# Performance work log

Hardware: AMD Instinct MI355X
Metric: run time of the kernel (lower is better)

## Reference

```python
import jax, jax.numpy as jnp
import numpy as np

N_SAMPLES = 32768
N_EVENTS = 16
WINDOW = 512
STEP = 256
N_FRAMES = 128          # n_samples // step_size
TOTAL_COEFFS = 16385    # n_samples // 2 + 1
N_COEFFS = 257          # window_size // 2 + 1
MIN_RES = 0.01


def max_norm(x):
    return x / (jnp.max(jnp.abs(x), axis=-1, keepdims=True) + 1e-8)


def linear_interp_last(x, out_size):
    """torch F.interpolate(mode='linear', align_corners=False) along last dim."""
    L = x.shape[-1]
    scale = L / out_size
    pos = (jnp.arange(out_size, dtype=jnp.float32) + 0.5) * scale - 0.5
    pos = jnp.clip(pos, 0.0, L - 1.0)
    i0 = jnp.floor(pos).astype(jnp.int32)
    i1 = jnp.minimum(i0 + 1, L - 1)
    w = pos - i0.astype(jnp.float32)
    return x[..., i0] * (1.0 - w) + x[..., i1] * w


def setup_inputs() -> dict:
    key = jax.random.key(0)
    k1, k2 = jax.random.split(key)
    x = jax.random.uniform(k1, (32, N_EVENTS, 533), dtype=jnp.float32)
    noise = jax.random.uniform(k2, (32, N_EVENTS, N_SAMPLES), dtype=jnp.float32)
    return {"x": x, "noise": noise}


def _forward(x, noise):
    x = jnp.clip(x, 0.0, 1.0)  # unit_activation

    # unpack
    means = x[..., 0:1] * 2.0 - 1.0                       # [B,E,1]
    stds = x[..., 1:2] * 0.1                              # [B,E,1]
    amps = x[..., 2:3]                                    # [B,E,1]
    res_mag = MIN_RES + (1.0 - MIN_RES) * x[..., 3:260]   # [B,E,257]
    freqs = (jnp.fft.rfftfreq(WINDOW) * np.pi).astype(jnp.float32)
    res_phase = x[..., 260:517] * (2.0 * np.pi) - np.pi + freqs  # [B,E,257]
    noise_coeff = x[..., 517:533]                         # [B,E,16]

    # ---- localized_noise ----
    rng = jnp.arange(N_SAMPLES, dtype=jnp.float32)
    mu = jnp.clip(means * N_SAMPLES, -(N_SAMPLES // 2), N_SAMPLES * 1.5)
    sigma = jnp.clip((1e-8 + stds) * N_SAMPLES, 0.0, N_SAMPLES - 1.0)
    logp = -0.5 * ((rng - mu) / sigma) ** 2 - jnp.log(sigma) - 0.5 * np.log(2.0 * np.pi)
    probs = max_norm(jnp.exp(logp))                       # [B,E,N]

    u = noise * 2.0 - 1.0                                 # uniform(-1,1)
    spec_shape = linear_interp_last(noise_coeff, TOTAL_COEFFS)  # [B,E,16385]
    nspec = jnp.fft.rfft(u, norm='ortho') * spec_shape
    nband = jnp.fft.irfft(nspec, n=N_SAMPLES, norm='ortho')
    atoms = probs * nband * amps                          # [B,E,N]

    # ---- resonance ----
    padded = jnp.pad(atoms, ((0, 0), (0, 0), (0, STEP)))
    idx = jnp.arange(N_FRAMES)[:, None] * STEP + jnp.arange(WINDOW)[None, :]
    frames = padded[..., idx]                             # [B,E,F,W]
    n = jnp.arange(WINDOW, dtype=jnp.float32)
    hamming = 0.54 - 0.46 * jnp.cos(2.0 * np.pi * n / WINDOW)  # periodic
    spec = jnp.fft.rfft(frames * hamming, norm='ortho')   # [B,E,F,257]

    # to_mag_and_phase
    re, im = spec.real, spec.imag
    mag = jnp.sqrt(re * re + im * im) + 1e-8              # [B,E,F,257]
    phase = (im / mag) * np.pi

    # mag recurrence m_t = mag_t + r * m_{t-1} (m_0 = mag_0) via scan over frames
    mag_t = jnp.moveaxis(mag, 2, 0)                       # [F,B,E,C]
    def step(carry, a):
        m = a + res_mag * carry
        return m, m
    _, ms = jax.lax.scan(step, jnp.zeros_like(mag_t[0]), mag_t)
    mags = jnp.moveaxis(ms, 0, 2)                         # [B,E,F,C]

    # phase: frame 0 unchanged, frames>=1 get + res_phase offset
    fmask = (jnp.arange(N_FRAMES) > 0).astype(phase.dtype)[None, None, :, None]
    phases = phase + fmask * res_phase[:, :, None, :]

    final = jax.lax.complex(mags * jnp.cos(phases), mags * jnp.sin(phases))
    res = jnp.fft.irfft(final, n=WINDOW, norm='ortho')    # [B,E,F,W]

    # overlap-add (hop = W/2), no window
    firsts, seconds = res[..., :STEP], res[..., STEP:]
    out = jnp.zeros(res.shape[:2] + (N_FRAMES + 1, STEP), res.dtype)
    out = out.at[:, :, :N_FRAMES].add(firsts).at[:, :, 1:].add(seconds)
    sig = out.reshape(out.shape[0], out.shape[1], -1)[..., :N_SAMPLES]  # [B,E,N]

    summed = jnp.sum(sig, axis=1, keepdims=True)          # [B,1,N]
    return max_norm(summed)


def reference(x, noise):
    return _forward(x, noise)
```

## Files before the change

kernel.cpp:

```cpp
#include <hip/hip_runtime.h>
#include <math.h>

#define PI_F 3.14159265358979323846f

__device__ __forceinline__ float2 cadd(float2 a, float2 b){ return make_float2(a.x+b.x, a.y+b.y); }
__device__ __forceinline__ float2 csub(float2 a, float2 b){ return make_float2(a.x-b.x, a.y-b.y); }
__device__ __forceinline__ float2 cmul(float2 a, float2 b){ return make_float2(a.x*b.x - a.y*b.y, a.x*b.y + a.y*b.x); }
__device__ __forceinline__ float2 cscale(float2 a, float s){ return make_float2(a.x*s, a.y*s); }
__device__ __forceinline__ float clip01(float v){ return fminf(fmaxf(v, 0.0f), 1.0f); }

__device__ __forceinline__ float uniformf(float v){
  return __int_as_float(__builtin_amdgcn_readfirstlane(__float_as_int(v)));
}

__device__ __forceinline__ int swz14(int p){ return p ^ (15 & ((p>>4) ^ (p>>8) ^ (p>>12))); }
__device__ __forceinline__ int swz8 (int p){ return p ^ ((p>>4) & 15); }

__device__ __forceinline__ int dr14(int k){
  unsigned x = __brev((unsigned)k) >> 18;
  return (int)(((x & 0x1555u) << 1) | ((x >> 1) & 0x1555u));
}
__device__ __forceinline__ int dr8(int k){
  unsigned x = __brev((unsigned)k) >> 24;
  return (int)(((x & 0x55u) << 1) | ((x >> 1) & 0x55u));
}

__device__ __forceinline__ void unpack_pair(float2 Zk, float2 Zm, float sn, float cs,
                                            float2& Uk, float2& Um) {
  float2 A  = make_float2(0.5f*(Zk.x+Zm.x), 0.5f*(Zk.y-Zm.y));
  float2 B  = make_float2(Zk.x-Zm.x, Zk.y+Zm.y);
  Uk = cadd(A, cmul(B, make_float2(-0.5f*sn, -0.5f*cs)));
  float2 Bm = make_float2(-B.x, B.y);
  Um = cadd(make_float2(A.x, -A.y), cmul(Bm, make_float2(-0.5f*sn, 0.5f*cs)));
}
__device__ __forceinline__ void repack_pair(float2 Vk, float2 Vm, float sn, float cs,
                                            float2& Wk, float2& Wm) {
  float2 P = make_float2(Vk.x+Vm.x, Vk.y-Vm.y);
  float2 Q = make_float2(Vk.x-Vm.x, Vk.y+Vm.y);
  Wk = cscale(cadd(P, cmul(Q, make_float2(-sn, cs))), 0.5f);
  float2 Qm = make_float2(-Q.x, Q.y);
  Wm = cscale(cadd(make_float2(P.x, -P.y), cmul(Qm, make_float2(-sn, -cs))), 0.5f);
}

__device__ __forceinline__ float sshape(int k, const float* ncs) {
  float pos = ((float)k + 0.5f) * (16.0f/16385.0f) - 0.5f;
  pos = fminf(fmaxf(pos, 0.0f), 15.0f);
  float fi = floorf(pos);
  int i0 = (int)fi;
  int i1 = min(i0 + 1, 15);
  float w = pos - fi;
  return ncs[i0]*(1.0f-w) + ncs[i1]*w;
}

#define LGKM() asm volatile("s_waitcnt lgkmcnt(0)" ::: "memory")

__device__ __forceinline__ void big_stage_fwd(float2* Cb, int u, int J, int lj) {
  int j = u & (J-1);
  int base = ((u >> lj) << (lj+2)) | j;
  float2 a0 = Cb[swz14(base)];
  float2 a1 = Cb[swz14(base+J)];
  float2 a2 = Cb[swz14(base+2*J)];
  float2 a3 = Cb[swz14(base+3*J)];
  float sn, cs; __sincosf((float)j * (-PI_F/(2.0f*(float)J)), &sn, &cs);
  float2 w1 = make_float2(cs, sn), w2 = cmul(w1,w1), w3 = cmul(w2,w1);
  float2 t0 = cadd(a0,a2), t1 = cadd(a1,a3), t2 = csub(a0,a2), t3 = csub(a1,a3);
  float2 mi = make_float2(t3.y, -t3.x);
  Cb[swz14(base)]     = cadd(t0,t1);
  Cb[swz14(base+J)]   = cmul(cadd(t2,mi), w1);
  Cb[swz14(base+2*J)] = cmul(csub(t0,t1), w2);
  Cb[swz14(base+3*J)] = cmul(csub(t2,mi), w3);
}
__device__ __forceinline__ void big_stage_inv(float2* Cb, int u, int J, int lj) {
  int j = u & (J-1);
  int base = ((u >> lj) << (lj+2)) | j;
  float sn, cs; __sincosf((float)j * (PI_F/(2.0f*(float)J)), &sn, &cs);
  float2 v1 = make_float2(cs, sn), v2 = cmul(v1,v1), v3 = cmul(v2,v1);
  float2 b0 = Cb[swz14(base)];
  float2 b1 = cmul(Cb[swz14(base+J)],   v1);
  float2 b2 = cmul(Cb[swz14(base+2*J)], v2);
  float2 b3 = cmul(Cb[swz14(base+3*J)], v3);
  float2 s02 = cadd(b0,b2), d02 = csub(b0,b2), s13 = cadd(b1,b3), d13 = csub(b1,b3);
  float2 id13 = make_float2(-d13.y, d13.x);
  Cb[swz14(base)]     = cadd(s02, s13);
  Cb[swz14(base+J)]   = cadd(d02, id13);
  Cb[swz14(base+2*J)] = csub(s02, s13);
  Cb[swz14(base+3*J)] = csub(d02, id13);
}
__device__ __forceinline__ void fr_stage_fwd(float2* row, int u, int J, int lj) {
  int j = u & (J-1);
  int base = ((u >> lj) << (lj+2)) | j;
  float2 a0 = row[swz8(base)];
  float2 a1 = row[swz8(base+J)];
  float2 a2 = row[swz8(base+2*J)];
  float2 a3 = row[swz8(base+3*J)];
  float sn, cs; __sincosf((float)j * (-PI_F/(2.0f*(float)J)), &sn, &cs);
  float2 w1 = make_float2(cs, sn), w2 = cmul(w1,w1), w3 = cmul(w2,w1);
  float2 t0 = cadd(a0,a2), t1 = cadd(a1,a3), t2 = csub(a0,a2), t3 = csub(a1,a3);
  float2 mi = make_float2(t3.y, -t3.x);
  row[swz8(base)]     = cadd(t0,t1);
  row[swz8(base+J)]   = cmul(cadd(t2,mi), w1);
  row[swz8(base+2*J)] = cmul(csub(t0,t1), w2);
  row[swz8(base+3*J)] = cmul(csub(t2,mi), w3);
}
__device__ __forceinline__ void fr_stage_inv(float2* row, int u, int J, int lj) {
  int j = u & (J-1);
  int base = ((u >> lj) << (lj+2)) | j;
  float sn, cs; __sincosf((float)j * (PI_F/(2.0f*(float)J)), &sn, &cs);
  float2 v1 = make_float2(cs, sn), v2 = cmul(v1,v1), v3 = cmul(v2,v1);
  float2 b0 = row[swz8(base)];
  float2 b1 = cmul(row[swz8(base+J)],   v1);
  float2 b2 = cmul(row[swz8(base+2*J)], v2);
  float2 b3 = cmul(row[swz8(base+3*J)], v3);
  float2 s02 = cadd(b0,b2), d02 = csub(b0,b2), s13 = cadd(b1,b3), d13 = csub(b1,b3);
  float2 id13 = make_float2(-d13.y, d13.x);
  row[swz8(base)]     = cadd(s02, s13);
  row[swz8(base+J)]   = cadd(d02, id13);
  row[swz8(base+2*J)] = csub(s02, s13);
  row[swz8(base+3*J)] = csub(d02, id13);
}

__global__ void __launch_bounds__(1024, 1)
atoms_zero(float* __restrict__ out) { out[blockIdx.x * 1024 + threadIdx.x] = 0.0f; }

__global__ void __launch_bounds__(1024, 4)
atoms_noise(const float* __restrict__ x, const float* __restrict__ noise,
            float2* __restrict__ nbout) {
  const int blk = blockIdx.x;
  const int t   = threadIdx.x;

  const float* xr = x + (size_t)blk * 533;
  const float* nr = noise + (size_t)blk * 32768;

  __shared__ float2 Cs[16384];
  __shared__ float  ncs[16];

  if (t < 16) ncs[t] = clip01(xr[517 + t]);

  {
    const float4* nr4 = (const float4*)nr;
    #pragma unroll
    for (int i2 = 0; i2 < 8; ++i2) {
      int m = t + (i2 << 10);
      float4 v4 = nr4[m];
      Cs[swz14(2*m)]   = make_float2(v4.x*2.0f-1.0f, v4.y*2.0f-1.0f);
      Cs[swz14(2*m+1)] = make_float2(v4.z*2.0f-1.0f, v4.w*2.0f-1.0f);
    }
  }
  __syncthreads();

  const int ub = ((t >> 6) << 8) + (t & 63);

  #pragma unroll
  for (int r = 0; r < 4; ++r) big_stage_fwd(Cs, ub + (r<<6), 4096, 12);
  __syncthreads();
  #pragma unroll
  for (int r = 0; r < 4; ++r) big_stage_fwd(Cs, ub + (r<<6), 1024, 10);
  __syncthreads();
  #pragma unroll
  for (int r = 0; r < 4; ++r) big_stage_fwd(Cs, ub + (r<<6), 256, 8);
  LGKM();
  #pragma unroll
  for (int r = 0; r < 4; ++r) big_stage_fwd(Cs, ub + (r<<6), 64, 6);
  LGKM();
  #pragma unroll
  for (int r = 0; r < 4; ++r) big_stage_fwd(Cs, ub + (r<<6), 16, 4);
  LGKM();
  #pragma unroll
  for (int r = 0; r < 4; ++r) big_stage_fwd(Cs, ub + (r<<6), 4, 2);
  LGKM();
  #pragma unroll
  for (int r = 0; r < 4; ++r) big_stage_fwd(Cs, ub + (r<<6), 1, 0);
  __syncthreads();

  {
    const float invM = 1.0f / 16384.0f;
    for (int k = t; k < 8192; k += 1024) {
      if (k == 0) {
        float2 Z0 = Cs[0];
        float U0 = Z0.x + Z0.y;
        float UM = Z0.x - Z0.y;
        float V0 = U0 * sshape(0, ncs) * invM;
        float VM = UM * sshape(16384, ncs) * invM;
        Cs[0] = make_float2(0.5f*(V0+VM), 0.5f*(V0-VM));
      } else {
        int pk = swz14(dr14(k));
        int pm = swz14(dr14(16384 - k));
        float2 Zk = Cs[pk], Zm = Cs[pm];
        float sn, cs; __sincosf((float)k * (PI_F / 16384.0f), &sn, &cs);
        float2 Uk, Um; unpack_pair(Zk, Zm, sn, cs, Uk, Um);
        float2 Vk = cscale(Uk, sshape(k, ncs) * invM);
        float2 Vm = cscale(Um, sshape(16384 - k, ncs) * invM);
        float2 Wk, Wm; repack_pair(Vk, Vm, sn, cs, Wk, Wm);
        Cs[pk] = Wk; Cs[pm] = Wm;
      }
    }
    if (t == 0) {
      int p = swz14(2);
      float2 Z = Cs[p];
      float2 U = make_float2(Z.x, -Z.y);
      float2 V = cscale(U, sshape(8192, ncs) * invM);
      Cs[p] = make_float2(V.x, -V.y);
    }
  }
  __syncthreads();

  #pragma unroll
  for (int r = 0; r < 4; ++r) big_stage_inv(Cs, ub + (r<<6), 1, 0);
  LGKM();
  #pragma unroll
  for (int r = 0; r < 4; ++r) big_stage_inv(Cs, ub + (r<<6), 4, 2);
  LGKM();
  #pragma unroll
  for (int r = 0; r < 4; ++r) big_stage_inv(Cs, ub + (r<<6), 16, 4);
  LGKM();
  #pragma unroll
  for (int r = 0; r < 4; ++r) big_stage_inv(Cs, ub + (r<<6), 64, 6);
  LGKM();
  #pragma unroll
  for (int r = 0; r < 4; ++r) big_stage_inv(Cs, ub + (r<<6), 256, 8);
  __syncthreads();
  #pragma unroll
  for (int r = 0; r < 4; ++r) big_stage_inv(Cs, ub + (r<<6), 1024, 10);
  __syncthreads();
  #pragma unroll
  for (int r = 0; r < 4; ++r) big_stage_inv(Cs, ub + (r<<6), 4096, 12);
  __syncthreads();

  float2* dst = nbout + ((size_t)blk << 14);
  #pragma unroll
  for (int ii = 0; ii < 16; ++ii) {
    int j = t + (ii << 10);
    dst[j] = Cs[swz14(j)];
  }
}

__global__ void __launch_bounds__(512, 2)
atoms_frames(const float* __restrict__ x, const float2* __restrict__ nband,
             float2* __restrict__ wsrows) {
  const int blk = blockIdx.x;
  const int t   = threadIdx.x;
  const int w   = t >> 6;
  const int l   = t & 63;

  const float* xr = x + (size_t)blk * 533;
  const float2* nbd = nband + ((size_t)blk << 14);
  float2* wsrow = wsrows + ((size_t)blk << 14);

  __shared__ float2 FR[8][256];
  __shared__ float  magb[8*257];
  __shared__ float  resmag[257], resphase[257], msarr[257];
  __shared__ float2 carrybuf[2][128];
  __shared__ float2 hamtab[256];

  const float xc0 = clip01(xr[0]);
  const float xc1 = clip01(xr[1]);
  const float amp = clip01(xr[2]);
  const float mean = xc0 * 2.0f - 1.0f;
  const float stdv = xc1 * 0.1f;
  float mu_v = fminf(fmaxf(mean * 32768.0f, -16384.0f), 49152.0f);
  float sigma = fminf(fmaxf((1e-8f + stdv) * 32768.0f, 0.0f), 32767.0f);
  float K_v = -logf(sigma) - 0.91893853320467274f;
  float invsig_v = 1.0f / sigma;
  float istar = fminf(fmaxf(roundf(mu_v), 0.0f), 32767.0f);
  float ds0 = (istar - mu_v) * invsig_v;
  float emax = __expf(-0.5f * ds0 * ds0 + K_v);
  const float mu     = uniformf(mu_v);
  const float invsig = uniformf(invsig_v);
  const float K      = uniformf(K_v);
  const float gscale = uniformf(amp / (emax + 1e-8f));

  if (t < 257) {
    resmag[t]   = 0.01f + 0.99f * clip01(xr[3 + t]);
    resphase[t] = clip01(xr[260 + t]) * (2.0f*PI_F) - PI_F + (float)t * (PI_F / 512.0f);
    msarr[t]    = 0.0f;
  }
  if (t < 128) carrybuf[0][t] = make_float2(0.0f, 0.0f);
  if (t < 256) {
    const float W512 = 2.0f * PI_F / 512.0f;
    float n0 = (float)(2*t);
    hamtab[t] = make_float2(0.54f - 0.46f*__cosf(n0*W512),
                            0.54f - 0.46f*__cosf((n0+1.0f)*W512));
  }
  __syncthreads();

  const float C2 = 0.044194173824159216f;
  const float F2 = 0.08838834764831845f;
  float2* row = FR[w];

  for (int g = 0; g < 16; ++g) {
    #pragma unroll
    for (int rep = 0; rep < 4; ++rep) {
      int slot = t + (rep << 9);
      int i = slot >> 8, j = slot & 255;
      int fg = (g << 3) + i;
      int cidx = (fg << 7) + j;
      float2 v = make_float2(0.0f, 0.0f);
      if (cidx < 16384) {
        float2 nb = nbd[cidx];
        float s0 = (float)(2*cidx);
        float d0 = (s0 - mu) * invsig;
        float d1 = (s0 + 1.0f - mu) * invsig;
        float2 h = hamtab[j];
        v = make_float2(__expf(-0.5f*d0*d0 + K) * gscale * nb.x * h.x,
                        __expf(-0.5f*d1*d1 + K) * gscale * nb.y * h.y);
      }
      FR[i][swz8(j)] = v;
    }
    __syncthreads();

    {
      fr_stage_fwd(row, l, 64, 6); LGKM();
      fr_stage_fwd(row, l, 16, 4); LGKM();
      fr_stage_fwd(row, l, 4, 2);  LGKM();
      fr_stage_fwd(row, l, 1, 0);  LGKM();

      if (l == 0) {
        float2 Z0 = row[0];
        float U0 = Z0.x + Z0.y, UM = Z0.x - Z0.y;
        magb[w*257 + 0]   = fabsf(U0)*C2 + 1e-8f;
        magb[w*257 + 256] = fabsf(UM)*C2 + 1e-8f;
        float2 Z = row[swz8(2)];
        magb[w*257 + 128] = sqrtf(Z.x*Z.x + Z.y*Z.y)*C2 + 1e-8f;
      } else {
        int pk = swz8(dr8(l)), pm = swz8(dr8(256 - l));
        float sn, cs; __sincosf((float)l * (PI_F/256.0f), &sn, &cs);
        float2 Uk, Um; unpack_pair(row[pk], row[pm], sn, cs, Uk, Um);
        magb[w*257 + l]     = sqrtf(Uk.x*Uk.x + Uk.y*Uk.y)*C2 + 1e-8f;
        magb[w*257 + 256-l] = sqrtf(Um.x*Um.x + Um.y*Um.y)*C2 + 1e-8f;
      }
      {
        const int kB = l + 64;
        int pk = swz8(dr8(kB)), pm = swz8(dr8(256 - kB));
        float sn, cs; __sincosf((float)kB * (PI_F/256.0f), &sn, &cs);
        float2 Uk, Um; unpack_pair(row[pk], row[pm], sn, cs, Uk, Um);
        magb[w*257 + kB]     = sqrtf(Uk.x*Uk.x + Uk.y*Uk.y)*C2 + 1e-8f;
        magb[w*257 + 256-kB] = sqrtf(Um.x*Um.x + Um.y*Um.y)*C2 + 1e-8f;
      }
    }
    __syncthreads();

    if (t < 257) {
      float rm = resmag[t], r = msarr[t];
      #pragma unroll
      for (int i = 0; i < 8; ++i) {
        float mg = magb[i*257 + t];
        r = fmaf(rm, r, mg);
        magb[i*257 + t] = r;
      }
      msarr[t] = r;
    }
    __syncthreads();

    {
      float fm = ((g << 3) + w > 0) ? 1.0f : 0.0f;
      if (l == 0) {
        float ms0 = magb[w*257 + 0]   * F2;
        float msM = magb[w*257 + 256] * F2;
        float V0 = ms0 * __cosf(fm*resphase[0]);
        float VM = msM * __cosf(fm*resphase[256]);
        row[0] = make_float2(0.5f*(V0+VM), 0.5f*(V0-VM));
        float2 Z = row[swz8(2)];
        float2 U = make_float2(Z.x, -Z.y);
        float mC = sqrtf(U.x*U.x + U.y*U.y)*C2 + 1e-8f;
        float pC = (U.y*C2/mC)*PI_F + fm*resphase[128];
        float msC = magb[w*257 + 128] * F2;
        float sC, cC; __sincosf(pC, &sC, &cC);
        row[swz8(2)] = make_float2(msC*cC, -(msC*sC));
      } else {
        int pk = swz8(dr8(l)), pm = swz8(dr8(256 - l));
        float sn, cs; __sincosf((float)l * (PI_F/256.0f), &sn, &cs);
        float2 Uk, Um; unpack_pair(row[pk], row[pm], sn, cs, Uk, Um);
        float mk = sqrtf(Uk.x*Uk.x + Uk.y*Uk.y)*C2 + 1e-8f;
        float mm = sqrtf(Um.x*Um.x + Um.y*Um.y)*C2 + 1e-8f;
        float p1 = (Uk.y*C2/mk)*PI_F + fm*resphase[l];
        float p2 = (Um.y*C2/mm)*PI_F + fm*resphase[256-l];
        float msk = magb[w*257 + l]     * F2;
        float msm = magb[w*257 + 256-l] * F2;
        float s1,c1,s2,c2; __sincosf(p1,&s1,&c1); __sincosf(p2,&s2,&c2);
        float2 Vk = make_float2(msk*c1, msk*s1);
        float2 Vm = make_float2(msm*c2, msm*s2);
        float2 Wk, Wm; repack_pair(Vk, Vm, sn, cs, Wk, Wm);
        row[pk] = Wk; row[pm] = Wm;
      }
      {
        const int kB = l + 64;
        int pk = swz8(dr8(kB)), pm = swz8(dr8(256 - kB));
        float sn, cs; __sincosf((float)kB * (PI_F/256.0f), &sn, &cs);
        float2 Uk, Um; unpack_pair(row[pk], row[pm], sn, cs, Uk, Um);
        float mk = sqrtf(Uk.x*Uk.x + Uk.y*Uk.y)*C2 + 1e-8f;
        float mm = sqrtf(Um.x*Um.x + Um.y*Um.y)*C2 + 1e-8f;
        float p1 = (Uk.y*C2/mk)*PI_F + fm*resphase[kB];
        float p2 = (Um.y*C2/mm)*PI_F + fm*resphase[256-kB];
        float msk = magb[w*257 + kB]     * F2;
        float msm = magb[w*257 + 256-kB] * F2;
        float s1,c1,s2,c2; __sincosf(p1,&s1,&c1); __sincosf(p2,&s2,&c2);
        float2 Vk = make_float2(msk*c1, msk*s1);
        float2 Vm = make_float2(msm*c2, msm*s2);
        float2 Wk, Wm; repack_pair(Vk, Vm, sn, cs, Wk, Wm);
        row[pk] = Wk; row[pm] = Wm;
      }
      LGKM();
      fr_stage_inv(row, l, 1, 0);  LGKM();
      fr_stage_inv(row, l, 4, 2);  LGKM();
      fr_stage_inv(row, l, 16, 4); LGKM();
      fr_stage_inv(row, l, 64, 6);
    }
    __syncthreads();

    #pragma unroll
    for (int rep = 0; rep < 2; ++rep) {
      int slot = t + (rep << 9);
      int i = slot >> 7, j = slot & 127;
      int fg = (g << 3) + i;
      float2 first  = FR[i][swz8(j)];
      float2 second = (i > 0) ? FR[i-1][swz8(128 + j)] : carrybuf[g & 1][j];
      wsrow[(fg << 7) + j] = cadd(first, second);
      if (i == 7) {
        carrybuf[(g & 1) ^ 1][j] = FR[7][swz8(128 + j)];
      }
    }
    __syncthreads();
  }
}

__global__ void __launch_bounds__(1024, 4)
atoms_main(const float* __restrict__ x, const float* __restrict__ noise,
           float* __restrict__ outacc, float2* __restrict__ wsbuf, int use_ws) {
  const int blk = blockIdx.x;
  const int b   = blk >> 4;
  const int t   = threadIdx.x;
  const int w   = t >> 6;
  const int l   = t & 63;

  const float* xr = x + (size_t)blk * 533;
  const float* nr = noise + (size_t)blk * 32768;

  __shared__ float2 Cs[16384];
  __shared__ float2 FR[8][256];
  __shared__ float  magb[8*257];
  __shared__ float  resmag[257], resphase[257], msarr[257];
  __shared__ float2 carrybuf[2][128];
  __shared__ float2 hamtab[256];
  __shared__ float  ncs[16];

  const float xc0 = clip01(xr[0]);
  const float xc1 = clip01(xr[1]);
  const float amp = clip01(xr[2]);
  const float mean = xc0 * 2.0f - 1.0f;
  const float stdv = xc1 * 0.1f;
  float mu_v = fminf(fmaxf(mean * 32768.0f, -16384.0f), 49152.0f);
  float sigma = fminf(fmaxf((1e-8f + stdv) * 32768.0f, 0.0f), 32767.0f);
  float K_v = -logf(sigma) - 0.91893853320467274f;
  float invsig_v = 1.0f / sigma;
  float istar = fminf(fmaxf(roundf(mu_v), 0.0f), 32767.0f);
  float ds0 = (istar - mu_v) * invsig_v;
  float emax = __expf(-0.5f * ds0 * ds0 + K_v);
  const float mu     = uniformf(mu_v);
  const float invsig = uniformf(invsig_v);
  const float K      = uniformf(K_v);
  const float gscale = uniformf(amp / (emax + 1e-8f));

  if (t < 257) {
    resmag[t]   = 0.01f + 0.99f * clip01(xr[3 + t]);
    resphase[t] = clip01(xr[260 + t]) * (2.0f*PI_F) - PI_F + (float)t * (PI_F / 512.0f);
    msarr[t]    = 0.0f;
  }
  if (t < 16)  ncs[t] = clip01(xr[517 + t]);
  if (t < 128) carrybuf[0][t] = make_float2(0.0f, 0.0f);
  if (t < 256) {
    const float W512 = 2.0f * PI_F / 512.0f;
    float n0 = (float)(2*t);
    hamtab[t] = make_float2(0.54f - 0.46f*__cosf(n0*W512),
                            0.54f - 0.46f*__cosf((n0+1.0f)*W512));
  }

  {
    const float4* nr4 = (const float4*)nr;
    #pragma unroll
    for (int i2 = 0; i2 < 8; ++i2) {
      int m = t + (i2 << 10);
      float4 v4 = nr4[m];
      Cs[swz14(2*m)]   = make_float2(v4.x*2.0f-1.0f, v4.y*2.0f-1.0f);
      Cs[swz14(2*m+1)] = make_float2(v4.z*2.0f-1.0f, v4.w*2.0f-1.0f);
    }
  }
  __syncthreads();

  const int ub = ((t >> 6) << 8) + (t & 63);

  #pragma unroll
  for (int r = 0; r < 4; ++r) big_stage_fwd(Cs, ub + (r<<6), 4096, 12);
  __syncthreads();
  #pragma unroll
  for (int r = 0; r < 4; ++r) big_stage_fwd(Cs, ub + (r<<6), 1024, 10);
  __syncthreads();
  #pragma unroll
  for (int r = 0; r < 4; ++r) big_stage_fwd(Cs, ub + (r<<6), 256, 8);
  LGKM();
  #pragma unroll
  for (int r = 0; r < 4; ++r) big_stage_fwd(Cs, ub + (r<<6), 64, 6);
  LGKM();
  #pragma unroll
  for (int r = 0; r < 4; ++r) big_stage_fwd(Cs, ub + (r<<6), 16, 4);
  LGKM();
  #pragma unroll
  for (int r = 0; r < 4; ++r) big_stage_fwd(Cs, ub + (r<<6), 4, 2);
  LGKM();
  #pragma unroll
  for (int r = 0; r < 4; ++r) big_stage_fwd(Cs, ub + (r<<6), 1, 0);
  __syncthreads();

  {
    const float invM = 1.0f / 16384.0f;
    for (int k = t; k < 8192; k += 1024) {
      if (k == 0) {
        float2 Z0 = Cs[0];
        float U0 = Z0.x + Z0.y;
        float UM = Z0.x - Z0.y;
        float V0 = U0 * sshape(0, ncs) * invM;
        float VM = UM * sshape(16384, ncs) * invM;
        Cs[0] = make_float2(0.5f*(V0+VM), 0.5f*(V0-VM));
      } else {
        int pk = swz14(dr14(k));
        int pm = swz14(dr14(16384 - k));
        float2 Zk = Cs[pk], Zm = Cs[pm];
        float sn, cs; __sincosf((float)k * (PI_F / 16384.0f), &sn, &cs);
        float2 Uk, Um; unpack_pair(Zk, Zm, sn, cs, Uk, Um);
        float2 Vk = cscale(Uk, sshape(k, ncs) * invM);
        float2 Vm = cscale(Um, sshape(16384 - k, ncs) * invM);
        float2 Wk, Wm; repack_pair(Vk, Vm, sn, cs, Wk, Wm);
        Cs[pk] = Wk; Cs[pm] = Wm;
      }
    }
    if (t == 0) {
      int p = swz14(2);
      float2 Z = Cs[p];
      float2 U = make_float2(Z.x, -Z.y);
      float2 V = cscale(U, sshape(8192, ncs) * (1.0f/16384.0f));
      Cs[p] = make_float2(V.x, -V.y);
    }
  }
  __syncthreads();

  #pragma unroll
  for (int r = 0; r < 4; ++r) big_stage_inv(Cs, ub + (r<<6), 1, 0);
  LGKM();
  #pragma unroll
  for (int r = 0; r < 4; ++r) big_stage_inv(Cs, ub + (r<<6), 4, 2);
  LGKM();
  #pragma unroll
  for (int r = 0; r < 4; ++r) big_stage_inv(Cs, ub + (r<<6), 16, 4);
  LGKM();
  #pragma unroll
  for (int r = 0; r < 4; ++r) big_stage_inv(Cs, ub + (r<<6), 64, 6);
  LGKM();
  #pragma unroll
  for (int r = 0; r < 4; ++r) big_stage_inv(Cs, ub + (r<<6), 256, 8);
  __syncthreads();
  #pragma unroll
  for (int r = 0; r < 4; ++r) big_stage_inv(Cs, ub + (r<<6), 1024, 10);
  __syncthreads();
  #pragma unroll
  for (int r = 0; r < 4; ++r) big_stage_inv(Cs, ub + (r<<6), 4096, 12);
  __syncthreads();

  const float C2 = 0.044194173824159216f;
  const float F2 = 0.08838834764831845f;
  float2* row = (w < 8) ? FR[w] : FR[0];
  float2* wsrow = use_ws ? (wsbuf + ((size_t)blk << 14)) : (float2*)0;

  for (int g = 0; g < 16; ++g) {
    #pragma unroll
    for (int rep = 0; rep < 2; ++rep) {
      int slot = t + (rep << 10);
      int i = slot >> 8, j = slot & 255;
      int fg = (g << 3) + i;
      int cidx = (fg << 7) + j;
      float2 v = make_float2(0.0f, 0.0f);
      if (cidx < 16384) {
        float2 nb = Cs[swz14(cidx)];
        float s0 = (float)(2*cidx);
        float d0 = (s0 - mu) * invsig;
        float d1 = (s0 + 1.0f - mu) * invsig;
        float2 h = hamtab[j];
        v = make_float2(__expf(-0.5f*d0*d0 + K) * gscale * nb.x * h.x,
                        __expf(-0.5f*d1*d1 + K) * gscale * nb.y * h.y);
      }
      FR[i][swz8(j)] = v;
    }
    __syncthreads();

    if (w < 8) {
      fr_stage_fwd(row, l, 64, 6); LGKM();
      fr_stage_fwd(row, l, 16, 4); LGKM();
      fr_stage_fwd(row, l, 4, 2);  LGKM();
      fr_stage_fwd(row, l, 1, 0);  LGKM();

      if (l == 0) {
        float2 Z0 = row[0];
        float U0 = Z0.x + Z0.y, UM = Z0.x - Z0.y;
        magb[w*257 + 0]   = fabsf(U0)*C2 + 1e-8f;
        magb[w*257 + 256] = fabsf(UM)*C2 + 1e-8f;
        float2 Z = row[swz8(2)];
        magb[w*257 + 128] = sqrtf(Z.x*Z.x + Z.y*Z.y)*C2 + 1e-8f;
      } else {
        int pk = swz8(dr8(l)), pm = swz8(dr8(256 - l));
        float sn, cs; __sincosf((float)l * (PI_F/256.0f), &sn, &cs);
        float2 Uk, Um; unpack_pair(row[pk], row[pm], sn, cs, Uk, Um);
        magb[w*257 + l]     = sqrtf(Uk.x*Uk.x + Uk.y*Uk.y)*C2 + 1e-8f;
        magb[w*257 + 256-l] = sqrtf(Um.x*Um.x + Um.y*Um.y)*C2 + 1e-8f;
      }
      {
        const int kB = l + 64;
        int pk = swz8(dr8(kB)), pm = swz8(dr8(256 - kB));
        float sn, cs; __sincosf((float)kB * (PI_F/256.0f), &sn, &cs);
        float2 Uk, Um; unpack_pair(row[pk], row[pm], sn, cs, Uk, Um);
        magb[w*257 + kB]     = sqrtf(Uk.x*Uk.x + Uk.y*Uk.y)*C2 + 1e-8f;
        magb[w*257 + 256-kB] = sqrtf(Um.x*Um.x + Um.y*Um.y)*C2 + 1e-8f;
      }
    }
    __syncthreads();

    if (t < 257) {
      float rm = resmag[t], r = msarr[t];
      #pragma unroll
      for (int i = 0; i < 8; ++i) {
        float mg = magb[i*257 + t];
        r = fmaf(rm, r, mg);
        magb[i*257 + t] = r;
      }
      msarr[t] = r;
    }
    __syncthreads();

    if (w < 8) {
      float fm = ((g << 3) + w > 0) ? 1.0f : 0.0f;
      if (l == 0) {
        float ms0 = magb[w*257 + 0]   * F2;
        float msM = magb[w*257 + 256] * F2;
        float V0 = ms0 * __cosf(fm*resphase[0]);
        float VM = msM * __cosf(fm*resphase[256]);
        row[0] = make_float2(0.5f*(V0+VM), 0.5f*(V0-VM));
        float2 Z = row[swz8(2)];
        float2 U = make_float2(Z.x, -Z.y);
        float mC = sqrtf(U.x*U.x + U.y*U.y)*C2 + 1e-8f;
        float pC = (U.y*C2/mC)*PI_F + fm*resphase[128];
        float msC = magb[w*257 + 128] * F2;
        float sC, cC; __sincosf(pC, &sC, &cC);
        row[swz8(2)] = make_float2(msC*cC, -(msC*sC));
      } else {
        int pk = swz8(dr8(l)), pm = swz8(dr8(256 - l));
        float sn, cs; __sincosf((float)l * (PI_F/256.0f), &sn, &cs);
        float2 Uk, Um; unpack_pair(row[pk], row[pm], sn, cs, Uk, Um);
        float mk = sqrtf(Uk.x*Uk.x + Uk.y*Uk.y)*C2 + 1e-8f;
        float mm = sqrtf(Um.x*Um.x + Um.y*Um.y)*C2 + 1e-8f;
        float p1 = (Uk.y*C2/mk)*PI_F + fm*resphase[l];
        float p2 = (Um.y*C2/mm)*PI_F + fm*resphase[256-l];
        float msk = magb[w*257 + l]     * F2;
        float msm = magb[w*257 + 256-l] * F2;
        float s1,c1,s2,c2; __sincosf(p1,&s1,&c1); __sincosf(p2,&s2,&c2);
        float2 Vk = make_float2(msk*c1, msk*s1);
        float2 Vm = make_float2(msm*c2, msm*s2);
        float2 Wk, Wm; repack_pair(Vk, Vm, sn, cs, Wk, Wm);
        row[pk] = Wk; row[pm] = Wm;
      }
      {
        const int kB = l + 64;
        int pk = swz8(dr8(kB)), pm = swz8(dr8(256 - kB));
        float sn, cs; __sincosf((float)kB * (PI_F/256.0f), &sn, &cs);
        float2 Uk, Um; unpack_pair(row[pk], row[pm], sn, cs, Uk, Um);
        float mk = sqrtf(Uk.x*Uk.x + Uk.y*Uk.y)*C2 + 1e-8f;
        float mm = sqrtf(Um.x*Um.x + Um.y*Um.y)*C2 + 1e-8f;
        float p1 = (Uk.y*C2/mk)*PI_F + fm*resphase[kB];
        float p2 = (Um.y*C2/mm)*PI_F + fm*resphase[256-kB];
        float msk = magb[w*257 + kB]     * F2;
        float msm = magb[w*257 + 256-kB] * F2;
        float s1,c1,s2,c2; __sincosf(p1,&s1,&c1); __sincosf(p2,&s2,&c2);
        float2 Vk = make_float2(msk*c1, msk*s1);
        float2 Vm = make_float2(msm*c2, msm*s2);
        float2 Wk, Wm; repack_pair(Vk, Vm, sn, cs, Wk, Wm);
        row[pk] = Wk; row[pm] = Wm;
      }
      LGKM();
      fr_stage_inv(row, l, 1, 0);  LGKM();
      fr_stage_inv(row, l, 4, 2);  LGKM();
      fr_stage_inv(row, l, 16, 4); LGKM();
      fr_stage_inv(row, l, 64, 6);
    }
    __syncthreads();

    {
      int i = t >> 7, j = t & 127;
      int fg = (g << 3) + i;
      float2 first  = FR[i][swz8(j)];
      float2 second = (i > 0) ? FR[i-1][swz8(128 + j)] : carrybuf[g & 1][j];
      float2 v = cadd(first, second);
      if (use_ws) {
        wsrow[(fg << 7) + j] = v;
      } else {
        float* dst = outacc + (size_t)b*32768 + (fg << 8) + 2*j;
        atomicAdd(dst,     v.x);
        atomicAdd(dst + 1, v.y);
      }
      if (i == 7) {
        carrybuf[(g & 1) ^ 1][j] = FR[7][swz8(128 + j)];
      }
    }
    __syncthreads();
  }
}

__global__ void __launch_bounds__(1024, 1)
atoms_sum_max(const float* __restrict__ ws, float* __restrict__ out, float* __restrict__ wmax) {
  int blk = blockIdx.x;
  int b = blk >> 3, seg = blk & 7, tid = threadIdx.x;
  const float* base = ws + (size_t)b*16*32768 + (size_t)seg*4096;
  float v[4]; float m = 0.0f;
  #pragma unroll
  for (int i = 0; i < 4; ++i) {
    int idx = (i << 10) + tid;
    float s = 0.0f;
    #pragma unroll
    for (int e = 0; e < 16; ++e) s += base[(size_t)e*32768 + idx];
    v[i] = s; m = fmaxf(m, fabsf(s));
  }
  float* op = out + (size_t)b*32768 + (seg << 12);
  #pragma unroll
  for (int i = 0; i < 4; ++i) op[(i<<10) + tid] = v[i];
  __shared__ float red[1024];
  red[tid] = m; __syncthreads();
  for (int s2 = 512; s2 > 0; s2 >>= 1) {
    if (tid < s2) red[tid] = fmaxf(red[tid], red[tid + s2]);
    __syncthreads();
  }
  if (tid == 0) wmax[blk] = red[0];
}

__global__ void __launch_bounds__(1024, 1)
atoms_scale(float* __restrict__ out, const float* __restrict__ wmax) {
  int blk = blockIdx.x;
  int b = blk >> 3, seg = blk & 7, tid = threadIdx.x;
  const float* wm = wmax + b*8;
  float m = fmaxf(fmaxf(fmaxf(wm[0],wm[1]), fmaxf(wm[2],wm[3])),
                  fmaxf(fmaxf(wm[4],wm[5]), fmaxf(wm[6],wm[7])));
  float inv = 1.0f / (m + 1e-8f);
  float* op = out + (size_t)b*32768 + (seg << 12);
  #pragma unroll
  for (int i = 0; i < 4; ++i) op[(i<<10) + tid] *= inv;
}

__global__ void __launch_bounds__(1024, 1)
atoms_norm(float* __restrict__ out) {
  const int b = blockIdx.x;
  const int tid = threadIdx.x;
  float* p = out + (size_t)b * 32768;
  __shared__ float red[1024];
  float m = 0.0f;
  for (int i = tid; i < 32768; i += 1024) m = fmaxf(m, fabsf(p[i]));
  red[tid] = m;
  __syncthreads();
  for (int s = 512; s > 0; s >>= 1) {
    if (tid < s) red[tid] = fmaxf(red[tid], red[tid + s]);
    __syncthreads();
  }
  const float inv = 1.0f / (red[0] + 1e-8f);
  for (int i = tid; i < 32768; i += 1024) p[i] = p[i] * inv;
}

extern "C" void kernel_launch(void* const* d_in, const int* in_sizes, int n_in,
                              void* d_out, int out_size, void* d_ws, size_t ws_size,
                              hipStream_t stream) {
  (void)in_sizes; (void)n_in; (void)out_size;
  const float* x     = (const float*)d_in[0];
  const float* noise = (const float*)d_in[1];
  float* out = (float*)d_out;

  const size_t rows_f    = 512ull * 32768ull;
  const size_t need_ws    = rows_f*4 + 4096;
  const size_t need_split = rows_f*4 + 4096 + rows_f*4;

  if (d_ws != nullptr && ws_size >= need_split) {
    float* ws    = (float*)d_ws;
    float* wmax  = ws + rows_f;
    float2* nbd  = (float2*)(ws + rows_f + 1024);
    atoms_noise <<<512, 1024, 0, stream>>>(x, noise, nbd);
    atoms_frames<<<512,  512, 0, stream>>>(x, nbd, (float2*)ws);
    atoms_sum_max<<<256, 1024, 0, stream>>>(ws, out, wmax);
    atoms_scale<<<256, 1024, 0, stream>>>(out, wmax);
  } else if (d_ws != nullptr && ws_size >= need_ws) {
    float* ws = (float*)d_ws;
    float* wmax = ws + rows_f;
    atoms_main<<<512, 1024, 0, stream>>>(x, noise, nullptr, (float2*)ws, 1);
    atoms_sum_max<<<256, 1024, 0, stream>>>(ws, out, wmax);
    atoms_scale<<<256, 1024, 0, stream>>>(out, wmax);
  } else {
    atoms_zero<<<1024, 1024, 0, stream>>>(out);
    atoms_main<<<512, 1024, 0, stream>>>(x, noise, out, nullptr, 0);
    atoms_norm<<<32, 1024, 0, stream>>>(out);
  }
}
```

Before: 274.2 us.

## Process two frames per wave in atoms_frames, halving group iterations and barriers

```diff
diff --git a/kernel.cpp b/kernel.cpp
--- a/kernel.cpp
+++ b/kernel.cpp
@@ -86,6 +86,52 @@
   Cb[swz14(base+2*J)] = csub(s02, s13);
   Cb[swz14(base+3*J)] = csub(d02, id13);
 }
+
+__device__ __forceinline__ void fr2_fwd(float2* rowA, float2* rowB, int l, int J, int lj) {
+  int j = l & (J-1);
+  int base = ((l >> lj) << (lj+2)) | j;
+  int i0 = swz8(base), i1 = swz8(base+J), i2 = swz8(base+2*J), i3 = swz8(base+3*J);
+  float2 a0=rowA[i0], a1=rowA[i1], a2=rowA[i2], a3=rowA[i3];
+  float2 b0=rowB[i0], b1=rowB[i1], b2=rowB[i2], b3=rowB[i3];
+  float sn, cs; __sincosf((float)j * (-PI_F/(2.0f*(float)J)), &sn, &cs);
+  float2 w1 = make_float2(cs, sn), w2 = cmul(w1,w1), w3 = cmul(w2,w1);
+  {
+    float2 t0=cadd(a0,a2), t1=cadd(a1,a3), t2=csub(a0,a2), t3=csub(a1,a3);
+    float2 mi=make_float2(t3.y,-t3.x);
+    rowA[i0]=cadd(t0,t1);          rowA[i1]=cmul(cadd(t2,mi),w1);
+    rowA[i2]=cmul(csub(t0,t1),w2); rowA[i3]=cmul(csub(t2,mi),w3);
+  }
+  {
+    float2 t0=cadd(b0,b2), t1=cadd(b1,b3), t2=csub(b0,b2), t3=csub(b1,b3);
+    float2 mi=make_float2(t3.y,-t3.x);
+    rowB[i0]=cadd(t0,t1);          rowB[i1]=cmul(cadd(t2,mi),w1);
+    rowB[i2]=cmul(csub(t0,t1),w2); rowB[i3]=cmul(csub(t2,mi),w3);
+  }
+}
+__device__ __forceinline__ void fr2_inv(float2* rowA, float2* rowB, int l, int J, int lj) {
+  int j = l & (J-1);
+  int base = ((l >> lj) << (lj+2)) | j;
+  int i0 = swz8(base), i1 = swz8(base+J), i2 = swz8(base+2*J), i3 = swz8(base+3*J);
+  float2 a0=rowA[i0], a1=rowA[i1], a2=rowA[i2], a3=rowA[i3];
+  float2 b0=rowB[i0], b1=rowB[i1], b2=rowB[i2], b3=rowB[i3];
+  float sn, cs; __sincosf((float)j * (PI_F/(2.0f*(float)J)), &sn, &cs);
+  float2 v1 = make_float2(cs, sn), v2 = cmul(v1,v1), v3 = cmul(v2,v1);
+  {
+    float2 c1=cmul(a1,v1), c2=cmul(a2,v2), c3=cmul(a3,v3);
+    float2 s02=cadd(a0,c2), d02=csub(a0,c2), s13=cadd(c1,c3), d13=csub(c1,c3);
+    float2 id13=make_float2(-d13.y,d13.x);
+    rowA[i0]=cadd(s02,s13); rowA[i1]=cadd(d02,id13);
+    rowA[i2]=csub(s02,s13); rowA[i3]=csub(d02,id13);
+  }
+  {
+    float2 c1=cmul(b1,v1), c2=cmul(b2,v2), c3=cmul(b3,v3);
+    float2 s02=cadd(b0,c2), d02=csub(b0,c2), s13=cadd(c1,c3), d13=csub(c1,c3);
+    float2 id13=make_float2(-d13.y,d13.x);
+    rowB[i0]=cadd(s02,s13); rowB[i1]=cadd(d02,id13);
+    rowB[i2]=csub(s02,s13); rowB[i3]=csub(d02,id13);
+  }
+}
+
 __device__ __forceinline__ void fr_stage_fwd(float2* row, int u, int J, int lj) {
   int j = u & (J-1);
   int base = ((u >> lj) << (lj+2)) | j;
@@ -234,7 +280,7 @@
   }
 }
 
-__global__ void __launch_bounds__(512, 2)
+__global__ void __launch_bounds__(512, 4)
 atoms_frames(const float* __restrict__ x, const float2* __restrict__ nband,
              float2* __restrict__ wsrows) {
   const int blk = blockIdx.x;
@@ -246,8 +292,9 @@
   const float2* nbd = nband + ((size_t)blk << 14);
   float2* wsrow = wsrows + ((size_t)blk << 14);
 
-  __shared__ float2 FR[8][256];
-  __shared__ float  magb[8*257];
+  __shared__ float2 FR[16][256];
+  __shared__ float  magb[16*257];
+  __shared__ float  phb[16*257];
   __shared__ float  resmag[257], resphase[257], msarr[257];
   __shared__ float2 carrybuf[2][128];
   __shared__ float2 hamtab[256];
@@ -285,138 +332,193 @@
 
   const float C2 = 0.044194173824159216f;
   const float F2 = 0.08838834764831845f;
-  float2* row = FR[w];
-
-  for (int g = 0; g < 16; ++g) {
+  const int iA = 2*w, iB = 2*w + 1;
+  float2* rowA = FR[iA];
+  float2* rowB = FR[iB];
+
+  for (int g = 0; g < 8; ++g) {
+    const int fgA = (g << 4) + iA;
+    const int fgB = fgA + 1;
+
     #pragma unroll
-    for (int rep = 0; rep < 4; ++rep) {
-      int slot = t + (rep << 9);
-      int i = slot >> 8, j = slot & 255;
-      int fg = (g << 3) + i;
-      int cidx = (fg << 7) + j;
-      float2 v = make_float2(0.0f, 0.0f);
-      if (cidx < 16384) {
-        float2 nb = nbd[cidx];
-        float s0 = (float)(2*cidx);
-        float d0 = (s0 - mu) * invsig;
-        float d1 = (s0 + 1.0f - mu) * invsig;
-        float2 h = hamtab[j];
-        v = make_float2(__expf(-0.5f*d0*d0 + K) * gscale * nb.x * h.x,
-                        __expf(-0.5f*d1*d1 + K) * gscale * nb.y * h.y);
-      }
-      FR[i][swz8(j)] = v;
-    }
-    __syncthreads();
-
-    {
-      fr_stage_fwd(row, l, 64, 6); LGKM();
-      fr_stage_fwd(row, l, 16, 4); LGKM();
-      fr_stage_fwd(row, l, 4, 2);  LGKM();
-      fr_stage_fwd(row, l, 1, 0);  LGKM();
-
-      if (l == 0) {
+    for (int r = 0; r < 4; ++r) {
+      int j = l + (r << 6);
+      float2 h = hamtab[j];
+      {
+        int cidx = (fgA << 7) + j;
+        float2 v = make_float2(0.0f, 0.0f);
+        if (cidx < 16384) {
+          float2 nb = nbd[cidx];
+          float s0 = (float)(2*cidx);
+          float d0 = (s0 - mu) * invsig;
+          float d1 = (s0 + 1.0f - mu) * invsig;
+          v = make_float2(__expf(-0.5f*d0*d0 + K) * gscale * nb.x * h.x,
+                          __expf(-0.5f*d1*d1 + K) * gscale * nb.y * h.y);
+        }
+        rowA[swz8(j)] = v;
+      }
+      {
+        int cidx = (fgB << 7) + j;
+        float2 v = make_float2(0.0f, 0.0f);
+        if (cidx < 16384) {
+          float2 nb = nbd[cidx];
+          float s0 = (float)(2*cidx);
+          float d0 = (s0 - mu) * invsig;
+          float d1 = (s0 + 1.0f - mu) * invsig;
+          v = make_float2(__expf(-0.5f*d0*d0 + K) * gscale * nb.x * h.x,
+                          __expf(-0.5f*d1*d1 + K) * gscale * nb.y * h.y);
+        }
+        rowB[swz8(j)] = v;
+      }
+    }
+    LGKM();
+
+    fr2_fwd(rowA, rowB, l, 64, 6); LGKM();
+    fr2_fwd(rowA, rowB, l, 16, 4); LGKM();
+    fr2_fwd(rowA, rowB, l, 4, 2);  LGKM();
+    fr2_fwd(rowA, rowB, l, 1, 0);  LGKM();
+
+    if (l == 0) {
+      #pragma unroll
+      for (int s = 0; s < 2; ++s) {
+        float2* row = s ? rowB : rowA;
+        int ii = s ? iB : iA;
         float2 Z0 = row[0];
         float U0 = Z0.x + Z0.y, UM = Z0.x - Z0.y;
-        magb[w*257 + 0]   = fabsf(U0)*C2 + 1e-8f;
-        magb[w*257 + 256] = fabsf(UM)*C2 + 1e-8f;
+        magb[ii*257 + 0]   = fabsf(U0)*C2 + 1e-8f;
+        magb[ii*257 + 256] = fabsf(UM)*C2 + 1e-8f;
         float2 Z = row[swz8(2)];
-        magb[w*257 + 128] = sqrtf(Z.x*Z.x + Z.y*Z.y)*C2 + 1e-8f;
+        float2 U = make_float2(Z.x, -Z.y);
+        float mC = sqrtf(U.x*U.x + U.y*U.y)*C2 + 1e-8f;
+        magb[ii*257 + 128] = mC;
+        phb[ii*257 + 128]  = (U.y*C2/mC)*PI_F;
+      }
+    } else {
+      int pk = swz8(dr8(l)), pm = swz8(dr8(256 - l));
+      float sn, cs; __sincosf((float)l * (PI_F/256.0f), &sn, &cs);
+      #pragma unroll
+      for (int s = 0; s < 2; ++s) {
+        float2* row = s ? rowB : rowA;
+        int ii = s ? iB : iA;
+        float2 Uk, Um; unpack_pair(row[pk], row[pm], sn, cs, Uk, Um);
+        float mk = sqrtf(Uk.x*Uk.x + Uk.y*Uk.y)*C2 + 1e-8f;
+        float mm = sqrtf(Um.x*Um.x + Um.y*Um.y)*C2 + 1e-8f;
+        magb[ii*257 + l]     = mk;
+        magb[ii*257 + 256-l] = mm;
+        phb[ii*257 + l]      = (Uk.y*C2/mk)*PI_F;
+        phb[ii*257 + 256-l]  = (Um.y*C2/mm)*PI_F;
+      }
+    }
+    {
+      const int kB = l + 64;
+      int pk = swz8(dr8(kB)), pm = swz8(dr8(256 - kB));
+      float sn, cs; __sincosf((float)kB * (PI_F/256.0f), &sn, &cs);
+      #pragma unroll
+      for (int s = 0; s < 2; ++s) {
+        float2* row = s ? rowB : rowA;
+        int ii = s ? iB : iA;
+        float2 Uk, Um; unpack_pair(row[pk], row[pm], sn, cs, Uk, Um);
+        float mk = sqrtf(Uk.x*Uk.x + Uk.y*Uk.y)*C2 + 1e-8f;
+        float mm = sqrtf(Um.x*Um.x + Um.y*Um.y)*C2 + 1e-8f;
+        magb[ii*257 + kB]     = mk;
+        magb[ii*257 + 256-kB] = mm;
+        phb[ii*257 + kB]      = (Uk.y*C2/mk)*PI_F;
+        phb[ii*257 + 256-kB]  = (Um.y*C2/mm)*PI_F;
+      }
+    }
+    __syncthreads();
+
+    if (t < 257) {
+      float rm = resmag[t], r = msarr[t];
+      float mg[16];
+      #pragma unroll
+      for (int i = 0; i < 16; ++i) mg[i] = magb[i*257 + t];
+      #pragma unroll
+      for (int i = 0; i < 16; ++i) {
+        r = fmaf(rm, r, mg[i]);
+        magb[i*257 + t] = r;
+      }
+      msarr[t] = r;
+    }
+    __syncthreads();
+
+    {
+      const float fmA = (fgA > 0) ? 1.0f : 0.0f;
+      if (l == 0) {
+        #pragma unroll
+        for (int s = 0; s < 2; ++s) {
+          float2* row = s ? rowB : rowA;
+          int ii = s ? iB : iA;
+          float fm = s ? 1.0f : fmA;
+          float ms0 = magb[ii*257 + 0]   * F2;
+          float msM = magb[ii*257 + 256] * F2;
+          float V0 = ms0 * __cosf(fm*resphase[0]);
+          float VM = msM * __cosf(fm*resphase[256]);
+          row[0] = make_float2(0.5f*(V0+VM), 0.5f*(V0-VM));
+          float msC = magb[ii*257 + 128] * F2;
+          float pC  = phb[ii*257 + 128] + fm*resphase[128];
+          float sC, cC; __sincosf(pC, &sC, &cC);
+          row[swz8(2)] = make_float2(msC*cC, -(msC*sC));
+        }
       } else {
         int pk = swz8(dr8(l)), pm = swz8(dr8(256 - l));
         float sn, cs; __sincosf((float)l * (PI_F/256.0f), &sn, &cs);
-        float2 Uk, Um; unpack_pair(row[pk], row[pm], sn, cs, Uk, Um);
-        magb[w*257 + l]     = sqrtf(Uk.x*Uk.x + Uk.y*Uk.y)*C2 + 1e-8f;
-        magb[w*257 + 256-l] = sqrtf(Um.x*Um.x + Um.y*Um.y)*C2 + 1e-8f;
+        float rp1 = resphase[l], rp2 = resphase[256-l];
+        #pragma unroll
+        for (int s = 0; s < 2; ++s) {
+          float2* row = s ? rowB : rowA;
+          int ii = s ? iB : iA;
+          float fm = s ? 1.0f : fmA;
+          float msk = magb[ii*257 + l]     * F2;
+          float msm = magb[ii*257 + 256-l] * F2;
+          float p1 = phb[ii*257 + l]     + fm*rp1;
+          float p2 = phb[ii*257 + 256-l] + fm*rp2;
+          float s1,c1,s2,c2; __sincosf(p1,&s1,&c1); __sincosf(p2,&s2,&c2);
+          float2 Vk = make_float2(msk*c1, msk*s1);
+          float2 Vm = make_float2(msm*c2, msm*s2);
+          float2 Wk, Wm; repack_pair(Vk, Vm, sn, cs, Wk, Wm);
+          row[pk] = Wk; row[pm] = Wm;
+        }
       }
       {
         const int kB = l + 64;
         int pk = swz8(dr8(kB)), pm = swz8(dr8(256 - kB));
         float sn, cs; __sincosf((float)kB * (PI_F/256.0f), &sn, &cs);
-        float2 Uk, Um; unpack_pair(row[pk], row[pm], sn, cs, Uk, Um);
-        magb[w*257 + kB]     = sqrtf(Uk.x*Uk.x + Uk.y*Uk.y)*C2 + 1e-8f;
-        magb[w*257 + 256-kB] = sqrtf(Um.x*Um.x + Um.y*Um.y)*C2 + 1e-8f;
-      }
-    }
-    __syncthreads();
-
-    if (t < 257) {
-      float rm = resmag[t], r = msarr[t];
-      #pragma unroll
-      for (int i = 0; i < 8; ++i) {
-        float mg = magb[i*257 + t];
-        r = fmaf(rm, r, mg);
-        magb[i*257 + t] = r;
-      }
-      msarr[t] = r;
-    }
-    __syncthreads();
-
-    {
-      float fm = ((g << 3) + w > 0) ? 1.0f : 0.0f;
-      if (l == 0) {
-        float ms0 = magb[w*257 + 0]   * F2;
-        float msM = magb[w*257 + 256] * F2;
-        float V0 = ms0 * __cosf(fm*resphase[0]);
-        float VM = msM * __cosf(fm*resphase[256]);
-        row[0] = make_float2(0.5f*(V0+VM), 0.5f*(V0-VM));
-        float2 Z = row[swz8(2)];
-        float2 U = make_float2(Z.x, -Z.y);
-        float mC = sqrtf(U.x*U.x + U.y*U.y)*C2 + 1e-8f;
-        float pC = (U.y*C2/mC)*PI_F + fm*resphase[128];
-        float msC = magb[w*257 + 128] * F2;
-        float sC, cC; __sincosf(pC, &sC, &cC);
-        row[swz8(2)] = make_float2(msC*cC, -(msC*sC));
-      } else {
-        int pk = swz8(dr8(l)), pm = swz8(dr8(256 - l));
-        float sn, cs; __sincosf((float)l * (PI_F/256.0f), &sn, &cs);
-        float2 Uk, Um; unpack_pair(row[pk], row[pm], sn, cs, Uk, Um);
-        float mk = sqrtf(Uk.x*Uk.x + Uk.y*Uk.y)*C2 + 1e-8f;
-        float mm = sqrtf(Um.x*Um.x + Um.y*Um.y)*C2 + 1e-8f;
-        float p1 = (Uk.y*C2/mk)*PI_F + fm*resphase[l];
-        float p2 = (Um.y*C2/mm)*PI_F + fm*resphase[256-l];
-        float msk = magb[w*257 + l]     * F2;
-        float msm = magb[w*257 + 256-l] * F2;
-        float s1,c1,s2,c2; __sincosf(p1,&s1,&c1); __sincosf(p2,&s2,&c2);
-        float2 Vk = make_float2(msk*c1, msk*s1);
-        float2 Vm = make_float2(msm*c2, msm*s2);
-        float2 Wk, Wm; repack_pair(Vk, Vm, sn, cs, Wk, Wm);
-        row[pk] = Wk; row[pm] = Wm;
-      }
-      {
-        const int kB = l + 64;
-        int pk = swz8(dr8(kB)), pm = swz8(dr8(256 - kB));
-        float sn, cs; __sincosf((float)kB * (PI_F/256.0f), &sn, &cs);
-        float2 Uk, Um; unpack_pair(row[pk], row[pm], sn, cs, Uk, Um);
-        float mk = sqrtf(Uk.x*Uk.x + Uk.y*Uk.y)*C2 + 1e-8f;
-        float mm = sqrtf(Um.x*Um.x + Um.y*Um.y)*C2 + 1e-8f;
-        float p1 = (Uk.y*C2/mk)*PI_F + fm*resphase[kB];
-        float p2 = (Um.y*C2/mm)*PI_F + fm*resphase[256-kB];
-        float msk = magb[w*257 + kB]     * F2;
-        float msm = magb[w*257 + 256-kB] * F2;
-        float s1,c1,s2,c2; __sincosf(p1,&s1,&c1); __sincosf(p2,&s2,&c2);
-        float2 Vk = make_float2(msk*c1, msk*s1);
-        float2 Vm = make_float2(msm*c2, msm*s2);
-        float2 Wk, Wm; repack_pair(Vk, Vm, sn, cs, Wk, Wm);
-        row[pk] = Wk; row[pm] = Wm;
+        float rp1 = resphase[kB], rp2 = resphase[256-kB];
+        #pragma unroll
+        for (int s = 0; s < 2; ++s) {
+          float2* row = s ? rowB : rowA;
+          int ii = s ? iB : iA;
+          float fm = s ? 1.0f : fmA;
+          float msk = magb[ii*257 + kB]     * F2;
+          float msm = magb[ii*257 + 256-kB] * F2;
+          float p1 = phb[ii*257 + kB]     + fm*rp1;
+          float p2 = phb[ii*257 + 256-kB] + fm*rp2;
+          float s1,c1,s2,c2; __sincosf(p1,&s1,&c1); __sincosf(p2,&s2,&c2);
+          float2 Vk = make_float2(msk*c1, msk*s1);
+          float2 Vm = make_float2(msm*c2, msm*s2);
+          float2 Wk, Wm; repack_pair(Vk, Vm, sn, cs, Wk, Wm);
+          row[pk] = Wk; row[pm] = Wm;
+        }
       }
       LGKM();
-      fr_stage_inv(row, l, 1, 0);  LGKM();
-      fr_stage_inv(row, l, 4, 2);  LGKM();
-      fr_stage_inv(row, l, 16, 4); LGKM();
-      fr_stage_inv(row, l, 64, 6);
+      fr2_inv(rowA, rowB, l, 1, 0);  LGKM();
+      fr2_inv(rowA, rowB, l, 4, 2);  LGKM();
+      fr2_inv(rowA, rowB, l, 16, 4); LGKM();
+      fr2_inv(rowA, rowB, l, 64, 6);
     }
     __syncthreads();
 
     #pragma unroll
-    for (int rep = 0; rep < 2; ++rep) {
+    for (int rep = 0; rep < 4; ++rep) {
       int slot = t + (rep << 9);
       int i = slot >> 7, j = slot & 127;
-      int fg = (g << 3) + i;
+      int fg = (g << 4) + i;
       float2 first  = FR[i][swz8(j)];
       float2 second = (i > 0) ? FR[i-1][swz8(128 + j)] : carrybuf[g & 1][j];
       wsrow[(fg << 7) + j] = cadd(first, second);
-      if (i == 7) {
-        carrybuf[(g & 1) ^ 1][j] = FR[7][swz8(128 + j)];
+      if (i == 15) {
+        carrybuf[(g & 1) ^ 1][j] = FR[15][swz8(128 + j)];
       }
     }
     __syncthreads();
```

New measurement: 337.8 us. 23.2% more time.
